# Kernel optimization log

Measured on AMD Instinct MI355X. Metric: run time of the kernel, lower is better.

Reference implementation:

```python
import jax, jax.numpy as jnp
import numpy as np

EPS = 1e-8

def _cosine_weights(keys, M, reverse=False):
    # keys: (bs, r, W); M: (bs, W, N) -> softmax over slots of cosine sim, shape (bs, r, N)
    kn = keys / (jnp.linalg.norm(keys, axis=-1, keepdims=True) + EPS)
    Mn = M / (jnp.linalg.norm(M, axis=1, keepdims=True) + EPS)
    dist = jnp.einsum('brw,bwn->brn', kn, Mn)
    if reverse:
        dist = -dist
    return jax.nn.softmax(dist, axis=2)

def setup_inputs() -> dict:
    key = jax.random.key(0)
    ks = jax.random.split(key, 8)
    bs, W, N, R = 128, 256, 2048, 4
    return {
        'k_r': jax.random.normal(ks[0], (bs, R * W), jnp.float32),
        'm_t': jax.random.normal(ks[1], (bs, W), jnp.float32),
        'e_t': jax.random.normal(ks[2], (bs, W), jnp.float32),
        'm_erased': jax.random.normal(ks[3], (bs, 1, W), jnp.float32),
        'memory': jax.random.uniform(ks[4], (bs, W, N), jnp.float32),
        'gW': jax.random.normal(ks[5], (1, 2 * W), jnp.float32) * 0.05,
        'gb': jnp.zeros((1,), jnp.float32),
        'oW': jax.random.normal(ks[6], (W, 2 * W), jnp.float32) * 0.05,
        'ob': jnp.zeros((W,), jnp.float32),
    }

def reference(k_r, m_t, e_t, m_erased, memory, gW, gb, oW, ob):
    bs, W, N = memory.shape
    R = k_r.shape[1] // W
    read_keys = jnp.tanh(k_r.reshape(bs, R, W))
    write_m = jnp.tanh(m_t.reshape(bs, 1, W))            # m_t candidate (bs,1,W)
    erase_vec = jax.nn.softmax(e_t.reshape(bs, 1, W), axis=2)
    # MixGate(write_m, m_erased)
    cat = jnp.concatenate([write_m, m_erased], axis=-1)  # (bs,1,2W)
    g = jax.nn.sigmoid(jnp.einsum('biw,ow->bio', cat, gW) + gb)  # (bs,1,1)
    gated = jnp.concatenate([g * write_m, (1.0 - g) * m_erased], axis=-1)
    write_key = jax.nn.relu(jnp.einsum('biw,ow->bio', gated, oW) + ob)  # (bs,1,W)
    # content weighting with reversed (dissimilarity) cosine
    write_wt = _cosine_weights(write_key, memory, reverse=True)  # (bs,1,N)
    # M = M * (1 - et^T wt) + mt^T wt
    reset_gate = 1.0 - jnp.einsum('biw,bin->bwn', erase_vec, write_wt)
    M_new = memory * reset_gate + jnp.einsum('biw,bin->bwn', write_m, write_wt)
    # read
    read_wt = _cosine_weights(read_keys, M_new)          # (bs,R,N)
    m_read = jnp.einsum('brn,bwn->brw', read_wt, M_new)  # (bs,R,W)
    return (m_read, M_new, read_wt)
```

## Files before the change

### kernel.cpp

```cpp
#include <hip/hip_runtime.h>
#include <math.h>

#define EPS 1e-8f
#define BS 128
#define W 256
#define N 2048
#define R 4

__device__ inline float wave_sum(float v) {
#pragma unroll
    for (int o = 32; o > 0; o >>= 1) v += __shfl_xor(v, o, 64);
    return v;
}
__device__ inline float wave_max(float v) {
#pragma unroll
    for (int o = 32; o > 0; o >>= 1) v = fmaxf(v, __shfl_xor(v, o, 64));
    return v;
}

__global__ void k_prep(const float* __restrict__ k_r, const float* __restrict__ m_t,
                       const float* __restrict__ e_t, const float* __restrict__ m_er,
                       const float* __restrict__ gW, const float* __restrict__ gb,
                       const float* __restrict__ oW, const float* __restrict__ ob,
                       float* __restrict__ wm_o, float* __restrict__ er_o,
                       float* __restrict__ knw_o, float* __restrict__ knr_o) {
    int b = blockIdx.x, t = threadIdx.x;
    int lane = t & 63, wid = t >> 6;
    __shared__ float red[4];
    __shared__ float gated[2 * W];
    __shared__ float wk_s[W];

    float wm = tanhf(m_t[b * W + t]);
    float me = m_er[b * W + t];
    wm_o[b * W + t] = wm;

    float e = e_t[b * W + t];
    float mx = wave_max(e);
    if (lane == 0) red[wid] = mx;
    __syncthreads();
    mx = fmaxf(fmaxf(red[0], red[1]), fmaxf(red[2], red[3]));
    __syncthreads();
    float ex = expf(e - mx);
    float s = wave_sum(ex);
    if (lane == 0) red[wid] = s;
    __syncthreads();
    s = red[0] + red[1] + red[2] + red[3];
    __syncthreads();
    er_o[b * W + t] = ex / s;

    float p = wm * gW[t] + me * gW[W + t];
    float ps = wave_sum(p);
    if (lane == 0) red[wid] = ps;
    __syncthreads();
    ps = red[0] + red[1] + red[2] + red[3] + gb[0];
    __syncthreads();
    float g = 1.0f / (1.0f + expf(-ps));
    gated[t] = g * wm;
    gated[W + t] = (1.0f - g) * me;
    __syncthreads();

    const float4* g4 = (const float4*)gated;
    float4 g0 = g4[lane];
    float4 g1 = g4[64 + lane];
    for (int i = 0; i < 64; i++) {
        int o = wid * 64 + i;
        const float4* orow = (const float4*)(oW + (size_t)o * 2 * W);
        float4 w0 = orow[lane];
        float4 w1 = orow[64 + lane];
        float pp = w0.x * g0.x + w0.y * g0.y + w0.z * g0.z + w0.w * g0.w
                 + w1.x * g1.x + w1.y * g1.y + w1.z * g1.z + w1.w * g1.w;
        pp = wave_sum(pp);
        if (lane == 0) wk_s[o] = fmaxf(pp + ob[o], 0.0f);
    }
    __syncthreads();
    float wk = wk_s[t];
    float ss = wave_sum(wk * wk);
    if (lane == 0) red[wid] = ss;
    __syncthreads();
    ss = red[0] + red[1] + red[2] + red[3];
    __syncthreads();
    knw_o[b * W + t] = wk / (sqrtf(ss) + EPS);

    for (int r = 0; r < R; r++) {
        float rk = tanhf(k_r[(b * R + r) * W + t]);
        float s2 = wave_sum(rk * rk);
        if (lane == 0) red[wid] = s2;
        __syncthreads();
        s2 = red[0] + red[1] + red[2] + red[3];
        __syncthreads();
        knr_o[(b * R + r) * W + t] = rk / (sqrtf(s2) + EPS);
    }
}

__global__ void k_wdist(const float* __restrict__ mem, const float* __restrict__ knw,
                        float* __restrict__ dist) {
    int b = blockIdx.y;
    int t = threadIdx.x;
    int n4 = blockIdx.x * 256 + t;
    __shared__ float k[W];
    k[t] = knw[b * W + t];
    __syncthreads();
    const float4* base = (const float4*)(mem + (size_t)b * W * N) + n4;
    float4 dot = make_float4(0.f, 0.f, 0.f, 0.f);
    float4 ss = make_float4(0.f, 0.f, 0.f, 0.f);
#pragma unroll 8
    for (int w = 0; w < W; w++) {
        float4 v = base[(size_t)w * (N / 4)];
        float kw = k[w];
        dot.x += kw * v.x; dot.y += kw * v.y; dot.z += kw * v.z; dot.w += kw * v.w;
        ss.x += v.x * v.x; ss.y += v.y * v.y; ss.z += v.z * v.z; ss.w += v.w * v.w;
    }
    float4 o;
    o.x = -(dot.x / (sqrtf(ss.x) + EPS));
    o.y = -(dot.y / (sqrtf(ss.y) + EPS));
    o.z = -(dot.z / (sqrtf(ss.z) + EPS));
    o.w = -(dot.w / (sqrtf(ss.w) + EPS));
    ((float4*)(dist + (size_t)b * N))[n4] = o;
}

__global__ void k_softmax_rows(float* __restrict__ io) {
    int row = blockIdx.x, t = threadIdx.x;
    int lane = t & 63, wid = t >> 6;
    float* p = io + (size_t)row * N;
    __shared__ float red[4];
    float v[8];
    float mx = -INFINITY;
#pragma unroll
    for (int k = 0; k < 8; k++) {
        v[k] = p[t + k * 256];
        mx = fmaxf(mx, v[k]);
    }
    mx = wave_max(mx);
    if (lane == 0) red[wid] = mx;
    __syncthreads();
    mx = fmaxf(fmaxf(red[0], red[1]), fmaxf(red[2], red[3]));
    __syncthreads();
    float s = 0.f;
#pragma unroll
    for (int k = 0; k < 8; k++) {
        v[k] = expf(v[k] - mx);
        s += v[k];
    }
    s = wave_sum(s);
    if (lane == 0) red[wid] = s;
    __syncthreads();
    s = red[0] + red[1] + red[2] + red[3];
    float inv = 1.0f / s;
#pragma unroll
    for (int k = 0; k < 8; k++) p[t + k * 256] = v[k] * inv;
}

__global__ void k_update(const float* __restrict__ mem, const float* __restrict__ wdist,
                         const float* __restrict__ er, const float* __restrict__ wm,
                         const float* __restrict__ knr,
                         float* __restrict__ Mnew, float* __restrict__ dist_r) {
    int b = blockIdx.y;
    int t = threadIdx.x;
    int lane = t & 63, wid = t >> 6;
    int n4 = blockIdx.x * 256 + t;
    __shared__ float se[W], sw[W];
    __shared__ float4 skT[W];
    __shared__ float red[4];
    se[t] = er[b * W + t];
    sw[t] = wm[b * W + t];
    const float* kb = knr + (size_t)b * R * W;
    skT[t] = make_float4(kb[t], kb[W + t], kb[2 * W + t], kb[3 * W + t]);

    const float4* drow4 = (const float4*)(wdist + (size_t)b * N);
    float4 a0 = drow4[t];
    float4 a1 = drow4[256 + t];
    float mx = fmaxf(fmaxf(fmaxf(a0.x, a0.y), fmaxf(a0.z, a0.w)),
                     fmaxf(fmaxf(a1.x, a1.y), fmaxf(a1.z, a1.w)));
    mx = wave_max(mx);
    if (lane == 0) red[wid] = mx;
    __syncthreads();
    mx = fmaxf(fmaxf(red[0], red[1]), fmaxf(red[2], red[3]));
    __syncthreads();
    float sm = expf(a0.x - mx) + expf(a0.y - mx) + expf(a0.z - mx) + expf(a0.w - mx)
             + expf(a1.x - mx) + expf(a1.y - mx) + expf(a1.z - mx) + expf(a1.w - mx);
    sm = wave_sum(sm);
    if (lane == 0) red[wid] = sm;
    __syncthreads();
    sm = red[0] + red[1] + red[2] + red[3];
    float inv = 1.0f / sm;
    float4 dmine = drow4[n4];
    float4 wt;
    wt.x = expf(dmine.x - mx) * inv;
    wt.y = expf(dmine.y - mx) * inv;
    wt.z = expf(dmine.z - mx) * inv;
    wt.w = expf(dmine.w - mx) * inv;

    const float4* mb = (const float4*)(mem + (size_t)b * W * N) + n4;
    float4* ob = (float4*)(Mnew + (size_t)b * W * N) + n4;
    float4 ssv = make_float4(0.f, 0.f, 0.f, 0.f);
    float4 d0 = make_float4(0.f, 0.f, 0.f, 0.f);
    float4 d1 = make_float4(0.f, 0.f, 0.f, 0.f);
    float4 d2 = make_float4(0.f, 0.f, 0.f, 0.f);
    float4 d3 = make_float4(0.f, 0.f, 0.f, 0.f);
#pragma unroll 4
    for (int w = 0; w < W; w++) {
        float4 v = mb[(size_t)w * (N / 4)];
        float ew = se[w], mw = sw[w];
        float4 mn;
        mn.x = v.x + wt.x * (mw - v.x * ew);
        mn.y = v.y + wt.y * (mw - v.y * ew);
        mn.z = v.z + wt.z * (mw - v.z * ew);
        mn.w = v.w + wt.w * (mw - v.w * ew);
        ob[(size_t)w * (N / 4)] = mn;
        ssv.x += mn.x * mn.x; ssv.y += mn.y * mn.y;
        ssv.z += mn.z * mn.z; ssv.w += mn.w * mn.w;
        float4 kv = skT[w];
        d0.x += kv.x * mn.x; d0.y += kv.x * mn.y; d0.z += kv.x * mn.z; d0.w += kv.x * mn.w;
        d1.x += kv.y * mn.x; d1.y += kv.y * mn.y; d1.z += kv.y * mn.z; d1.w += kv.y * mn.w;
        d2.x += kv.z * mn.x; d2.y += kv.z * mn.y; d2.z += kv.z * mn.z; d2.w += kv.z * mn.w;
        d3.x += kv.w * mn.x; d3.y += kv.w * mn.y; d3.z += kv.w * mn.z; d3.w += kv.w * mn.w;
    }
    float4 ivn;
    ivn.x = 1.0f / (sqrtf(ssv.x) + EPS);
    ivn.y = 1.0f / (sqrtf(ssv.y) + EPS);
    ivn.z = 1.0f / (sqrtf(ssv.z) + EPS);
    ivn.w = 1.0f / (sqrtf(ssv.w) + EPS);
    float4* dr = (float4*)(dist_r + (size_t)b * R * N);
    dr[0 * (N / 4) + n4] = make_float4(d0.x * ivn.x, d0.y * ivn.y, d0.z * ivn.z, d0.w * ivn.w);
    dr[1 * (N / 4) + n4] = make_float4(d1.x * ivn.x, d1.y * ivn.y, d1.z * ivn.z, d1.w * ivn.w);
    dr[2 * (N / 4) + n4] = make_float4(d2.x * ivn.x, d2.y * ivn.y, d2.z * ivn.z, d2.w * ivn.w);
    dr[3 * (N / 4) + n4] = make_float4(d3.x * ivn.x, d3.y * ivn.y, d3.z * ivn.z, d3.w * ivn.w);
}

__global__ void k_mread(const float* __restrict__ Mnew, const float* __restrict__ rwt_g,
                        float* __restrict__ m_read) {
    int b = blockIdx.y;
    int w0 = blockIdx.x * 64;
    int t = threadIdx.x;
    int lane = t & 63, wid = t >> 6;
    int half = wid & 1, rowgrp = wid >> 1;
    int fbase = half * 256 + lane;

    float4 rw[R][4];
#pragma unroll
    for (int r = 0; r < R; r++) {
        const float4* rrow = (const float4*)(rwt_g + ((size_t)b * R + r) * N);
#pragma unroll
        for (int k = 0; k < 4; k++) rw[r][k] = rrow[fbase + k * 64];
    }

    __shared__ float part[64][2][4];
    const float* Mb = Mnew + (size_t)b * W * N;
#pragma unroll 2
    for (int wi = 0; wi < 32; wi++) {
        int wl = rowgrp * 32 + wi;
        const float4* mrow = (const float4*)(Mb + (size_t)(w0 + wl) * N);
        float4 v[4];
#pragma unroll
        for (int k = 0; k < 4; k++) v[k] = mrow[fbase + k * 64];
        float a0 = 0.f, a1 = 0.f, a2 = 0.f, a3 = 0.f;
#pragma unroll
        for (int k = 0; k < 4; k++) {
            a0 += rw[0][k].x * v[k].x + rw[0][k].y * v[k].y + rw[0][k].z * v[k].z + rw[0][k].w * v[k].w;
            a1 += rw[1][k].x * v[k].x + rw[1][k].y * v[k].y + rw[1][k].z * v[k].z + rw[1][k].w * v[k].w;
            a2 += rw[2][k].x * v[k].x + rw[2][k].y * v[k].y + rw[2][k].z * v[k].z + rw[2][k].w * v[k].w;
            a3 += rw[3][k].x * v[k].x + rw[3][k].y * v[k].y + rw[3][k].z * v[k].z + rw[3][k].w * v[k].w;
        }
        a0 = wave_sum(a0);
        a1 = wave_sum(a1);
        a2 = wave_sum(a2);
        a3 = wave_sum(a3);
        if (lane == 0) {
            part[wl][half][0] = a0;
            part[wl][half][1] = a1;
            part[wl][half][2] = a2;
            part[wl][half][3] = a3;
        }
    }
    __syncthreads();
    int w = t >> 2, r = t & 3;
    float sres = part[w][0][r] + part[w][1][r];
    m_read[((size_t)b * R + r) * W + w0 + w] = sres;
}

extern "C" void kernel_launch(void* const* d_in, const int* in_sizes, int n_in,
                              void* d_out, int out_size, void* d_ws, size_t ws_size,
                              hipStream_t stream) {
    const float* k_r  = (const float*)d_in[0];
    const float* m_t  = (const float*)d_in[1];
    const float* e_t  = (const float*)d_in[2];
    const float* m_er = (const float*)d_in[3];
    const float* mem  = (const float*)d_in[4];
    const float* gW   = (const float*)d_in[5];
    const float* gb   = (const float*)d_in[6];
    const float* oW   = (const float*)d_in[7];
    const float* ob   = (const float*)d_in[8];

    float* out = (float*)d_out;
    float* m_read = out;
    float* Mnew   = out + (size_t)BS * R * W;
    float* rwt    = out + (size_t)BS * R * W + (size_t)BS * W * N;

    float* ws  = (float*)d_ws;
    float* wm  = ws;
    float* er  = ws + (size_t)BS * W;
    float* knw = ws + (size_t)2 * BS * W;
    float* knr = ws + (size_t)3 * BS * W;
    float* wdist = ws + (size_t)3 * BS * W + (size_t)BS * R * W;

    k_prep<<<BS, 256, 0, stream>>>(k_r, m_t, e_t, m_er, gW, gb, oW, ob, wm, er, knw, knr);
    k_wdist<<<dim3(2, BS), 256, 0, stream>>>(mem, knw, wdist);
    k_update<<<dim3(2, BS), 256, 0, stream>>>(mem, wdist, er, wm, knr, Mnew, rwt);
    k_softmax_rows<<<BS * R, 256, 0, stream>>>(rwt);
    k_mread<<<dim3(4, BS), 256, 0, stream>>>(Mnew, rwt, m_read);
}
```

Before: 259.2 us.

## Split W reduction across two thread halves in wdist and update kernels

```diff
diff --git a/kernel.cpp b/kernel.cpp
--- a/kernel.cpp
+++ b/kernel.cpp
@@ -92,30 +92,42 @@
     }
 }
 
-__global__ void k_wdist(const float* __restrict__ mem, const float* __restrict__ knw,
-                        float* __restrict__ dist) {
+__global__ void __launch_bounds__(256, 2)
+k_wdist(const float* __restrict__ mem, const float* __restrict__ knw,
+        float* __restrict__ dist) {
     int b = blockIdx.y;
     int t = threadIdx.x;
-    int n4 = blockIdx.x * 256 + t;
+    int half = t >> 7, c = t & 127;
+    int n4 = blockIdx.x * 128 + c;
     __shared__ float k[W];
+    __shared__ float4 pdot[128], pss[128];
     k[t] = knw[b * W + t];
     __syncthreads();
     const float4* base = (const float4*)(mem + (size_t)b * W * N) + n4;
     float4 dot = make_float4(0.f, 0.f, 0.f, 0.f);
     float4 ss = make_float4(0.f, 0.f, 0.f, 0.f);
+    int w0 = half * 128;
 #pragma unroll 8
-    for (int w = 0; w < W; w++) {
+    for (int i = 0; i < 128; i++) {
+        int w = w0 + i;
         float4 v = base[(size_t)w * (N / 4)];
         float kw = k[w];
         dot.x += kw * v.x; dot.y += kw * v.y; dot.z += kw * v.z; dot.w += kw * v.w;
         ss.x += v.x * v.x; ss.y += v.y * v.y; ss.z += v.z * v.z; ss.w += v.w * v.w;
     }
-    float4 o;
-    o.x = -(dot.x / (sqrtf(ss.x) + EPS));
-    o.y = -(dot.y / (sqrtf(ss.y) + EPS));
-    o.z = -(dot.z / (sqrtf(ss.z) + EPS));
-    o.w = -(dot.w / (sqrtf(ss.w) + EPS));
-    ((float4*)(dist + (size_t)b * N))[n4] = o;
+    if (half == 0) { pdot[c] = dot; pss[c] = ss; }
+    __syncthreads();
+    if (half == 1) {
+        float4 od = pdot[c], os = pss[c];
+        dot.x += od.x; dot.y += od.y; dot.z += od.z; dot.w += od.w;
+        ss.x += os.x; ss.y += os.y; ss.z += os.z; ss.w += os.w;
+        float4 o;
+        o.x = -(dot.x / (sqrtf(ss.x) + EPS));
+        o.y = -(dot.y / (sqrtf(ss.y) + EPS));
+        o.z = -(dot.z / (sqrtf(ss.z) + EPS));
+        o.w = -(dot.w / (sqrtf(ss.w) + EPS));
+        ((float4*)(dist + (size_t)b * N))[n4] = o;
+    }
 }
 
 __global__ void k_softmax_rows(float* __restrict__ io) {
@@ -150,17 +162,20 @@
     for (int k = 0; k < 8; k++) p[t + k * 256] = v[k] * inv;
 }
 
-__global__ void k_update(const float* __restrict__ mem, const float* __restrict__ wdist,
-                         const float* __restrict__ er, const float* __restrict__ wm,
-                         const float* __restrict__ knr,
-                         float* __restrict__ Mnew, float* __restrict__ dist_r) {
+__global__ void __launch_bounds__(256, 2)
+k_update(const float* __restrict__ mem, const float* __restrict__ wdist,
+         const float* __restrict__ er, const float* __restrict__ wm,
+         const float* __restrict__ knr,
+         float* __restrict__ Mnew, float* __restrict__ dist_r) {
     int b = blockIdx.y;
     int t = threadIdx.x;
     int lane = t & 63, wid = t >> 6;
-    int n4 = blockIdx.x * 256 + t;
+    int half = t >> 7, c = t & 127;
+    int n4 = blockIdx.x * 128 + c;
     __shared__ float se[W], sw[W];
     __shared__ float4 skT[W];
     __shared__ float red[4];
+    __shared__ float4 pd0[128], pd1[128], pd2[128], pd3[128], pssv[128];
     se[t] = er[b * W + t];
     sw[t] = wm[b * W + t];
     const float* kb = knr + (size_t)b * R * W;
@@ -197,8 +212,10 @@
     float4 d1 = make_float4(0.f, 0.f, 0.f, 0.f);
     float4 d2 = make_float4(0.f, 0.f, 0.f, 0.f);
     float4 d3 = make_float4(0.f, 0.f, 0.f, 0.f);
-#pragma unroll 4
-    for (int w = 0; w < W; w++) {
+    int w0 = half * 128;
+#pragma unroll 8
+    for (int i = 0; i < 128; i++) {
+        int w = w0 + i;
         float4 v = mb[(size_t)w * (N / 4)];
         float ew = se[w], mw = sw[w];
         float4 mn;
@@ -215,20 +232,33 @@
         d2.x += kv.z * mn.x; d2.y += kv.z * mn.y; d2.z += kv.z * mn.z; d2.w += kv.z * mn.w;
         d3.x += kv.w * mn.x; d3.y += kv.w * mn.y; d3.z += kv.w * mn.z; d3.w += kv.w * mn.w;
     }
-    float4 ivn;
-    ivn.x = 1.0f / (sqrtf(ssv.x) + EPS);
-    ivn.y = 1.0f / (sqrtf(ssv.y) + EPS);
-    ivn.z = 1.0f / (sqrtf(ssv.z) + EPS);
-    ivn.w = 1.0f / (sqrtf(ssv.w) + EPS);
-    float4* dr = (float4*)(dist_r + (size_t)b * R * N);
-    dr[0 * (N / 4) + n4] = make_float4(d0.x * ivn.x, d0.y * ivn.y, d0.z * ivn.z, d0.w * ivn.w);
-    dr[1 * (N / 4) + n4] = make_float4(d1.x * ivn.x, d1.y * ivn.y, d1.z * ivn.z, d1.w * ivn.w);
-    dr[2 * (N / 4) + n4] = make_float4(d2.x * ivn.x, d2.y * ivn.y, d2.z * ivn.z, d2.w * ivn.w);
-    dr[3 * (N / 4) + n4] = make_float4(d3.x * ivn.x, d3.y * ivn.y, d3.z * ivn.z, d3.w * ivn.w);
-}
-
-__global__ void k_mread(const float* __restrict__ Mnew, const float* __restrict__ rwt_g,
-                        float* __restrict__ m_read) {
+    if (half == 0) {
+        pd0[c] = d0; pd1[c] = d1; pd2[c] = d2; pd3[c] = d3; pssv[c] = ssv;
+    }
+    __syncthreads();
+    if (half == 1) {
+        float4 q;
+        q = pd0[c]; d0.x += q.x; d0.y += q.y; d0.z += q.z; d0.w += q.w;
+        q = pd1[c]; d1.x += q.x; d1.y += q.y; d1.z += q.z; d1.w += q.w;
+        q = pd2[c]; d2.x += q.x; d2.y += q.y; d2.z += q.z; d2.w += q.w;
+        q = pd3[c]; d3.x += q.x; d3.y += q.y; d3.z += q.z; d3.w += q.w;
+        q = pssv[c]; ssv.x += q.x; ssv.y += q.y; ssv.z += q.z; ssv.w += q.w;
+        float4 ivn;
+        ivn.x = 1.0f / (sqrtf(ssv.x) + EPS);
+        ivn.y = 1.0f / (sqrtf(ssv.y) + EPS);
+        ivn.z = 1.0f / (sqrtf(ssv.z) + EPS);
+        ivn.w = 1.0f / (sqrtf(ssv.w) + EPS);
+        float4* dr = (float4*)(dist_r + (size_t)b * R * N);
+        dr[0 * (N / 4) + n4] = make_float4(d0.x * ivn.x, d0.y * ivn.y, d0.z * ivn.z, d0.w * ivn.w);
+        dr[1 * (N / 4) + n4] = make_float4(d1.x * ivn.x, d1.y * ivn.y, d1.z * ivn.z, d1.w * ivn.w);
+        dr[2 * (N / 4) + n4] = make_float4(d2.x * ivn.x, d2.y * ivn.y, d2.z * ivn.z, d2.w * ivn.w);
+        dr[3 * (N / 4) + n4] = make_float4(d3.x * ivn.x, d3.y * ivn.y, d3.z * ivn.z, d3.w * ivn.w);
+    }
+}
+
+__global__ void __launch_bounds__(256, 2)
+k_mread(const float* __restrict__ Mnew, const float* __restrict__ rwt_g,
+        float* __restrict__ m_read) {
     int b = blockIdx.y;
     int w0 = blockIdx.x * 64;
     int t = threadIdx.x;
@@ -246,7 +276,7 @@
 
     __shared__ float part[64][2][4];
     const float* Mb = Mnew + (size_t)b * W * N;
-#pragma unroll 2
+#pragma unroll 4
     for (int wi = 0; wi < 32; wi++) {
         int wl = rowgrp * 32 + wi;
         const float4* mrow = (const float4*)(Mb + (size_t)(w0 + wl) * N);
@@ -304,8 +334,8 @@
     float* wdist = ws + (size_t)3 * BS * W + (size_t)BS * R * W;
 
     k_prep<<<BS, 256, 0, stream>>>(k_r, m_t, e_t, m_er, gW, gb, oW, ob, wm, er, knw, knr);
-    k_wdist<<<dim3(2, BS), 256, 0, stream>>>(mem, knw, wdist);
-    k_update<<<dim3(2, BS), 256, 0, stream>>>(mem, wdist, er, wm, knr, Mnew, rwt);
+    k_wdist<<<dim3(4, BS), 256, 0, stream>>>(mem, knw, wdist);
+    k_update<<<dim3(4, BS), 256, 0, stream>>>(mem, wdist, er, wm, knr, Mnew, rwt);
     k_softmax_rows<<<BS * R, 256, 0, stream>>>(rwt);
     k_mread<<<dim3(4, BS), 256, 0, stream>>>(Mnew, rwt, m_read);
 }
```

Measured after the change: 267.9 us. 3.4% more time.

## Compute read distances algebraically from memory moments, fusing update and read

Applied to the files above, without the earlier changes.

```diff
diff --git a/kernel.cpp b/kernel.cpp
--- a/kernel.cpp
+++ b/kernel.cpp
@@ -5,7 +5,10 @@
 #define BS 128
 #define W 256
 #define N 2048
+#define N4 (N / 4)
 #define R 4
+
+using v4f = float __attribute__((ext_vector_type(4)));
 
 __device__ inline float wave_sum(float v) {
 #pragma unroll
@@ -16,6 +19,28 @@
 #pragma unroll
     for (int o = 32; o > 0; o >>= 1) v = fmaxf(v, __shfl_xor(v, o, 64));
     return v;
+}
+__device__ inline float block_sum(float v, volatile float* red, int lane, int wid) {
+    v = wave_sum(v);
+    if (lane == 0) red[wid] = v;
+    __syncthreads();
+    v = red[0] + red[1] + red[2] + red[3];
+    __syncthreads();
+    return v;
+}
+__device__ inline float block_max(float v, volatile float* red, int lane, int wid) {
+    v = wave_max(v);
+    if (lane == 0) red[wid] = v;
+    __syncthreads();
+    v = fmaxf(fmaxf(red[0], red[1]), fmaxf(red[2], red[3]));
+    __syncthreads();
+    return v;
+}
+__device__ inline void fma4s(float4& a, float s, const float4& v) {
+    a.x += s * v.x; a.y += s * v.y; a.z += s * v.z; a.w += s * v.w;
+}
+__device__ inline void fma44(float4& a, const float4& u, const float4& v) {
+    a.x += u.x * v.x; a.y += u.y * v.y; a.z += u.z * v.z; a.w += u.w * v.w;
 }
 
 __global__ void k_prep(const float* __restrict__ k_r, const float* __restrict__ m_t,
@@ -23,7 +48,8 @@
                        const float* __restrict__ gW, const float* __restrict__ gb,
                        const float* __restrict__ oW, const float* __restrict__ ob,
                        float* __restrict__ wm_o, float* __restrict__ er_o,
-                       float* __restrict__ knw_o, float* __restrict__ knr_o) {
+                       float* __restrict__ knw_o, float* __restrict__ knr_o,
+                       float* __restrict__ c0_o) {
     int b = blockIdx.x, t = threadIdx.x;
     int lane = t & 63, wid = t >> 6;
     __shared__ float red[4];
@@ -35,25 +61,16 @@
     wm_o[b * W + t] = wm;
 
     float e = e_t[b * W + t];
-    float mx = wave_max(e);
-    if (lane == 0) red[wid] = mx;
-    __syncthreads();
-    mx = fmaxf(fmaxf(red[0], red[1]), fmaxf(red[2], red[3]));
-    __syncthreads();
+    float mx = block_max(e, red, lane, wid);
     float ex = expf(e - mx);
-    float s = wave_sum(ex);
-    if (lane == 0) red[wid] = s;
-    __syncthreads();
-    s = red[0] + red[1] + red[2] + red[3];
-    __syncthreads();
+    float s = block_sum(ex, red, lane, wid);
     er_o[b * W + t] = ex / s;
 
+    float pw = block_sum(wm * wm, red, lane, wid);
+    if (t == 0) c0_o[b * 5 + 4] = pw;
+
     float p = wm * gW[t] + me * gW[W + t];
-    float ps = wave_sum(p);
-    if (lane == 0) red[wid] = ps;
-    __syncthreads();
-    ps = red[0] + red[1] + red[2] + red[3] + gb[0];
-    __syncthreads();
+    float ps = block_sum(p, red, lane, wid) + gb[0];
     float g = 1.0f / (1.0f + expf(-ps));
     gated[t] = g * wm;
     gated[W + t] = (1.0f - g) * me;
@@ -74,208 +91,277 @@
     }
     __syncthreads();
     float wk = wk_s[t];
-    float ss = wave_sum(wk * wk);
-    if (lane == 0) red[wid] = ss;
-    __syncthreads();
-    ss = red[0] + red[1] + red[2] + red[3];
-    __syncthreads();
+    float ss = block_sum(wk * wk, red, lane, wid);
     knw_o[b * W + t] = wk / (sqrtf(ss) + EPS);
 
     for (int r = 0; r < R; r++) {
         float rk = tanhf(k_r[(b * R + r) * W + t]);
-        float s2 = wave_sum(rk * rk);
-        if (lane == 0) red[wid] = s2;
-        __syncthreads();
-        s2 = red[0] + red[1] + red[2] + red[3];
-        __syncthreads();
-        knr_o[(b * R + r) * W + t] = rk / (sqrtf(s2) + EPS);
-    }
-}
-
-__global__ void k_wdist(const float* __restrict__ mem, const float* __restrict__ knw,
-                        float* __restrict__ dist) {
-    int b = blockIdx.y;
+        float s2 = block_sum(rk * rk, red, lane, wid);
+        float kn = rk / (sqrtf(s2) + EPS);
+        knr_o[(b * R + r) * W + t] = kn;
+        float c0 = block_sum(kn * wm, red, lane, wid);
+        if (t == 0) c0_o[b * 5 + r] = c0;
+    }
+}
+
+__global__ void __launch_bounds__(256, 2)
+k_moments(const float* __restrict__ mem, const float* __restrict__ knw_g,
+          const float* __restrict__ er_g, const float* __restrict__ wm_g,
+          const float* __restrict__ knr_g, float4* __restrict__ scr) {
+    int b = blockIdx.y, bx = blockIdx.x;
     int t = threadIdx.x;
-    int n4 = blockIdx.x * 256 + t;
-    __shared__ float k[W];
-    k[t] = knw[b * W + t];
-    __syncthreads();
+    int half = t >> 7, c = t & 127;
+    int n4 = bx * 128 + c;
+    __shared__ float knw_s[W], er_s[W], wm_s[W], knr_s[R * W];
+    __shared__ float4 comb[128 * 7];
+
+    knw_s[t] = knw_g[b * W + t];
+    er_s[t]  = er_g[b * W + t];
+    wm_s[t]  = wm_g[b * W + t];
+#pragma unroll
+    for (int r = 0; r < R; r++) knr_s[r * W + t] = knr_g[(b * R + r) * W + t];
+    __syncthreads();
+
+    float4 acc[14];
+#pragma unroll
+    for (int j = 0; j < 14; j++) acc[j] = make_float4(0.f, 0.f, 0.f, 0.f);
+
     const float4* base = (const float4*)(mem + (size_t)b * W * N) + n4;
-    float4 dot = make_float4(0.f, 0.f, 0.f, 0.f);
-    float4 ss = make_float4(0.f, 0.f, 0.f, 0.f);
-#pragma unroll 8
-    for (int w = 0; w < W; w++) {
-        float4 v = base[(size_t)w * (N / 4)];
-        float kw = k[w];
-        dot.x += kw * v.x; dot.y += kw * v.y; dot.z += kw * v.z; dot.w += kw * v.w;
-        ss.x += v.x * v.x; ss.y += v.y * v.y; ss.z += v.z * v.z; ss.w += v.w * v.w;
-    }
-    float4 o;
-    o.x = -(dot.x / (sqrtf(ss.x) + EPS));
-    o.y = -(dot.y / (sqrtf(ss.y) + EPS));
-    o.z = -(dot.z / (sqrtf(ss.z) + EPS));
-    o.w = -(dot.w / (sqrtf(ss.w) + EPS));
-    ((float4*)(dist + (size_t)b * N))[n4] = o;
-}
-
-__global__ void k_softmax_rows(float* __restrict__ io) {
-    int row = blockIdx.x, t = threadIdx.x;
-    int lane = t & 63, wid = t >> 6;
-    float* p = io + (size_t)row * N;
-    __shared__ float red[4];
-    float v[8];
-    float mx = -INFINITY;
-#pragma unroll
-    for (int k = 0; k < 8; k++) {
-        v[k] = p[t + k * 256];
-        mx = fmaxf(mx, v[k]);
-    }
-    mx = wave_max(mx);
-    if (lane == 0) red[wid] = mx;
-    __syncthreads();
-    mx = fmaxf(fmaxf(red[0], red[1]), fmaxf(red[2], red[3]));
-    __syncthreads();
-    float s = 0.f;
-#pragma unroll
-    for (int k = 0; k < 8; k++) {
-        v[k] = expf(v[k] - mx);
-        s += v[k];
-    }
-    s = wave_sum(s);
-    if (lane == 0) red[wid] = s;
-    __syncthreads();
-    s = red[0] + red[1] + red[2] + red[3];
-    float inv = 1.0f / s;
-#pragma unroll
-    for (int k = 0; k < 8; k++) p[t + k * 256] = v[k] * inv;
-}
-
-__global__ void k_update(const float* __restrict__ mem, const float* __restrict__ wdist,
-                         const float* __restrict__ er, const float* __restrict__ wm,
-                         const float* __restrict__ knr,
-                         float* __restrict__ Mnew, float* __restrict__ dist_r) {
-    int b = blockIdx.y;
+    int w0 = half * 128;
+#pragma unroll 4
+    for (int i = 0; i < 128; i++) {
+        int w = w0 + i;
+        float4 v = base[(size_t)w * N4];
+        float e = er_s[w], m = wm_s[w], kw = knw_s[w];
+        float4 ev;
+        ev.x = e * v.x; ev.y = e * v.y; ev.z = e * v.z; ev.w = e * v.w;
+        fma4s(acc[0], kw, v);
+        fma44(acc[1], v, v);
+        fma44(acc[2], ev, v);
+        fma44(acc[3], ev, ev);
+        fma4s(acc[4], m, v);
+        fma4s(acc[5], m, ev);
+        fma4s(acc[6], knr_s[w], v);
+        fma4s(acc[7], knr_s[W + w], v);
+        fma4s(acc[8], knr_s[2 * W + w], v);
+        fma4s(acc[9], knr_s[3 * W + w], v);
+        fma4s(acc[10], knr_s[w], ev);
+        fma4s(acc[11], knr_s[W + w], ev);
+        fma4s(acc[12], knr_s[2 * W + w], ev);
+        fma4s(acc[13], knr_s[3 * W + w], ev);
+    }
+
+    if (half == 0) {
+#pragma unroll
+        for (int j = 0; j < 7; j++) comb[c * 7 + j] = acc[j];
+    }
+    __syncthreads();
+    if (half == 1) {
+#pragma unroll
+        for (int j = 0; j < 7; j++) {
+            float4 q = comb[c * 7 + j];
+            q.x += acc[j].x; q.y += acc[j].y; q.z += acc[j].z; q.w += acc[j].w;
+            scr[((size_t)(b * 14 + j)) * N4 + n4] = q;
+        }
+    }
+    __syncthreads();
+    if (half == 0) {
+#pragma unroll
+        for (int j = 0; j < 7; j++) comb[c * 7 + j] = acc[7 + j];
+    }
+    __syncthreads();
+    if (half == 1) {
+#pragma unroll
+        for (int j = 0; j < 7; j++) {
+            float4 q = comb[c * 7 + j];
+            q.x += acc[7 + j].x; q.y += acc[7 + j].y; q.z += acc[7 + j].z; q.w += acc[7 + j].w;
+            scr[((size_t)(b * 14 + 7 + j)) * N4 + n4] = q;
+        }
+    }
+}
+
+__global__ void k_weights(const float4* __restrict__ scr, const float* __restrict__ c0_g,
+                          float* __restrict__ wwt_g, float* __restrict__ rwt_out,
+                          float* __restrict__ C_g) {
+    int b = blockIdx.y, pair = blockIdx.x;
     int t = threadIdx.x;
     int lane = t & 63, wid = t >> 6;
-    int n4 = blockIdx.x * 256 + t;
-    __shared__ float se[W], sw[W];
-    __shared__ float4 skT[W];
     __shared__ float red[4];
-    se[t] = er[b * W + t];
-    sw[t] = wm[b * W + t];
-    const float* kb = knr + (size_t)b * R * W;
-    skT[t] = make_float4(kb[t], kb[W + t], kb[2 * W + t], kb[3 * W + t]);
-
-    const float4* drow4 = (const float4*)(wdist + (size_t)b * N);
-    float4 a0 = drow4[t];
-    float4 a1 = drow4[256 + t];
-    float mx = fmaxf(fmaxf(fmaxf(a0.x, a0.y), fmaxf(a0.z, a0.w)),
-                     fmaxf(fmaxf(a1.x, a1.y), fmaxf(a1.z, a1.w)));
-    mx = wave_max(mx);
-    if (lane == 0) red[wid] = mx;
-    __syncthreads();
-    mx = fmaxf(fmaxf(red[0], red[1]), fmaxf(red[2], red[3]));
-    __syncthreads();
-    float sm = expf(a0.x - mx) + expf(a0.y - mx) + expf(a0.z - mx) + expf(a0.w - mx)
-             + expf(a1.x - mx) + expf(a1.y - mx) + expf(a1.z - mx) + expf(a1.w - mx);
-    sm = wave_sum(sm);
-    if (lane == 0) red[wid] = sm;
-    __syncthreads();
-    sm = red[0] + red[1] + red[2] + red[3];
-    float inv = 1.0f / sm;
-    float4 dmine = drow4[n4];
-    float4 wt;
-    wt.x = expf(dmine.x - mx) * inv;
-    wt.y = expf(dmine.y - mx) * inv;
-    wt.z = expf(dmine.z - mx) * inv;
-    wt.w = expf(dmine.w - mx) * inv;
-
-    const float4* mb = (const float4*)(mem + (size_t)b * W * N) + n4;
-    float4* ob = (float4*)(Mnew + (size_t)b * W * N) + n4;
-    float4 ssv = make_float4(0.f, 0.f, 0.f, 0.f);
-    float4 d0 = make_float4(0.f, 0.f, 0.f, 0.f);
-    float4 d1 = make_float4(0.f, 0.f, 0.f, 0.f);
-    float4 d2 = make_float4(0.f, 0.f, 0.f, 0.f);
-    float4 d3 = make_float4(0.f, 0.f, 0.f, 0.f);
-#pragma unroll 4
-    for (int w = 0; w < W; w++) {
-        float4 v = mb[(size_t)w * (N / 4)];
-        float ew = se[w], mw = sw[w];
-        float4 mn;
-        mn.x = v.x + wt.x * (mw - v.x * ew);
-        mn.y = v.y + wt.y * (mw - v.y * ew);
-        mn.z = v.z + wt.z * (mw - v.z * ew);
-        mn.w = v.w + wt.w * (mw - v.w * ew);
-        ob[(size_t)w * (N / 4)] = mn;
-        ssv.x += mn.x * mn.x; ssv.y += mn.y * mn.y;
-        ssv.z += mn.z * mn.z; ssv.w += mn.w * mn.w;
-        float4 kv = skT[w];
-        d0.x += kv.x * mn.x; d0.y += kv.x * mn.y; d0.z += kv.x * mn.z; d0.w += kv.x * mn.w;
-        d1.x += kv.y * mn.x; d1.y += kv.y * mn.y; d1.z += kv.y * mn.z; d1.w += kv.y * mn.w;
-        d2.x += kv.z * mn.x; d2.y += kv.z * mn.y; d2.z += kv.z * mn.z; d2.w += kv.z * mn.w;
-        d3.x += kv.w * mn.x; d3.y += kv.w * mn.y; d3.z += kv.w * mn.z; d3.w += kv.w * mn.w;
-    }
-    float4 ivn;
-    ivn.x = 1.0f / (sqrtf(ssv.x) + EPS);
-    ivn.y = 1.0f / (sqrtf(ssv.y) + EPS);
-    ivn.z = 1.0f / (sqrtf(ssv.z) + EPS);
-    ivn.w = 1.0f / (sqrtf(ssv.w) + EPS);
-    float4* dr = (float4*)(dist_r + (size_t)b * R * N);
-    dr[0 * (N / 4) + n4] = make_float4(d0.x * ivn.x, d0.y * ivn.y, d0.z * ivn.z, d0.w * ivn.w);
-    dr[1 * (N / 4) + n4] = make_float4(d1.x * ivn.x, d1.y * ivn.y, d1.z * ivn.z, d1.w * ivn.w);
-    dr[2 * (N / 4) + n4] = make_float4(d2.x * ivn.x, d2.y * ivn.y, d2.z * ivn.z, d2.w * ivn.w);
-    dr[3 * (N / 4) + n4] = make_float4(d3.x * ivn.x, d3.y * ivn.y, d3.z * ivn.z, d3.w * ivn.w);
-}
-
-__global__ void k_mread(const float* __restrict__ Mnew, const float* __restrict__ rwt_g,
-                        float* __restrict__ m_read) {
+
+    const float4* S0 = scr + (size_t)(b * 14) * N4;
+    float4 s1a = S0[t],        ssa = S0[N4 + t];
+    float4 s1b = S0[256 + t],  ssb = S0[N4 + 256 + t];
+
+    float4 da, db;
+    da.x = -(s1a.x / (sqrtf(ssa.x) + EPS)); da.y = -(s1a.y / (sqrtf(ssa.y) + EPS));
+    da.z = -(s1a.z / (sqrtf(ssa.z) + EPS)); da.w = -(s1a.w / (sqrtf(ssa.w) + EPS));
+    db.x = -(s1b.x / (sqrtf(ssb.x) + EPS)); db.y = -(s1b.y / (sqrtf(ssb.y) + EPS));
+    db.z = -(s1b.z / (sqrtf(ssb.z) + EPS)); db.w = -(s1b.w / (sqrtf(ssb.w) + EPS));
+
+    float m8 = fmaxf(fmaxf(fmaxf(da.x, da.y), fmaxf(da.z, da.w)),
+                     fmaxf(fmaxf(db.x, db.y), fmaxf(db.z, db.w)));
+    float mx = block_max(m8, red, lane, wid);
+    float4 ea, eb;
+    ea.x = expf(da.x - mx); ea.y = expf(da.y - mx); ea.z = expf(da.z - mx); ea.w = expf(da.w - mx);
+    eb.x = expf(db.x - mx); eb.y = expf(db.y - mx); eb.z = expf(db.z - mx); eb.w = expf(db.w - mx);
+    float s8 = ea.x + ea.y + ea.z + ea.w + eb.x + eb.y + eb.z + eb.w;
+    float Z = block_sum(s8, red, lane, wid);
+    float inv = 1.0f / Z;
+    float4 ua, ub;
+    ua.x = ea.x * inv; ua.y = ea.y * inv; ua.z = ea.z * inv; ua.w = ea.w * inv;
+    ub.x = eb.x * inv; ub.y = eb.y * inv; ub.z = eb.z * inv; ub.w = eb.w * inv;
+    if (pair == 0) {
+        ((float4*)(wwt_g + (size_t)b * N))[t] = ua;
+        ((float4*)(wwt_g + (size_t)b * N))[256 + t] = ub;
+    }
+
+    float4 q1a = S0[2 * N4 + t], q2a = S0[3 * N4 + t], p0a = S0[4 * N4 + t], p1a = S0[5 * N4 + t];
+    float4 q1b = S0[2 * N4 + 256 + t], q2b = S0[3 * N4 + 256 + t],
+           p0b = S0[4 * N4 + 256 + t], p1b = S0[5 * N4 + 256 + t];
+    float pw = c0_g[b * 5 + 4];
+
+    float4 dena, denb;
+    {
+        dena.x = sqrtf(ssa.x + ua.x * (2.f * p0a.x - 2.f * q1a.x) + ua.x * ua.x * (q2a.x - 2.f * p1a.x + pw)) + EPS;
+        dena.y = sqrtf(ssa.y + ua.y * (2.f * p0a.y - 2.f * q1a.y) + ua.y * ua.y * (q2a.y - 2.f * p1a.y + pw)) + EPS;
+        dena.z = sqrtf(ssa.z + ua.z * (2.f * p0a.z - 2.f * q1a.z) + ua.z * ua.z * (q2a.z - 2.f * p1a.z + pw)) + EPS;
+        dena.w = sqrtf(ssa.w + ua.w * (2.f * p0a.w - 2.f * q1a.w) + ua.w * ua.w * (q2a.w - 2.f * p1a.w + pw)) + EPS;
+        denb.x = sqrtf(ssb.x + ub.x * (2.f * p0b.x - 2.f * q1b.x) + ub.x * ub.x * (q2b.x - 2.f * p1b.x + pw)) + EPS;
+        denb.y = sqrtf(ssb.y + ub.y * (2.f * p0b.y - 2.f * q1b.y) + ub.y * ub.y * (q2b.y - 2.f * p1b.y + pw)) + EPS;
+        denb.z = sqrtf(ssb.z + ub.z * (2.f * p0b.z - 2.f * q1b.z) + ub.z * ub.z * (q2b.z - 2.f * p1b.z + pw)) + EPS;
+        denb.w = sqrtf(ssb.w + ub.w * (2.f * p0b.w - 2.f * q1b.w) + ub.w * ub.w * (q2b.w - 2.f * p1b.w + pw)) + EPS;
+    }
+
+#pragma unroll
+    for (int rr = 0; rr < 2; rr++) {
+        int r = pair * 2 + rr;
+        float c0 = c0_g[b * 5 + r];
+        float4 t0a = S0[(6 + r) * N4 + t], t1a = S0[(10 + r) * N4 + t];
+        float4 t0b = S0[(6 + r) * N4 + 256 + t], t1b = S0[(10 + r) * N4 + 256 + t];
+        float4 dra, drb;
+        dra.x = (t0a.x + ua.x * (c0 - t1a.x)) / dena.x;
+        dra.y = (t0a.y + ua.y * (c0 - t1a.y)) / dena.y;
+        dra.z = (t0a.z + ua.z * (c0 - t1a.z)) / dena.z;
+        dra.w = (t0a.w + ua.w * (c0 - t1a.w)) / dena.w;
+        drb.x = (t0b.x + ub.x * (c0 - t1b.x)) / denb.x;
+        drb.y = (t0b.y + ub.y * (c0 - t1b.y)) / denb.y;
+        drb.z = (t0b.z + ub.z * (c0 - t1b.z)) / denb.z;
+        drb.w = (t0b.w + ub.w * (c0 - t1b.w)) / denb.w;
+
+        float rm = fmaxf(fmaxf(fmaxf(dra.x, dra.y), fmaxf(dra.z, dra.w)),
+                         fmaxf(fmaxf(drb.x, drb.y), fmaxf(drb.z, drb.w)));
+        float rmx = block_max(rm, red, lane, wid);
+        float4 ra, rb;
+        ra.x = expf(dra.x - rmx); ra.y = expf(dra.y - rmx);
+        ra.z = expf(dra.z - rmx); ra.w = expf(dra.w - rmx);
+        rb.x = expf(drb.x - rmx); rb.y = expf(drb.y - rmx);
+        rb.z = expf(drb.z - rmx); rb.w = expf(drb.w - rmx);
+        float rs = ra.x + ra.y + ra.z + ra.w + rb.x + rb.y + rb.z + rb.w;
+        float RZ = block_sum(rs, red, lane, wid);
+        float rinv = 1.0f / RZ;
+        ra.x *= rinv; ra.y *= rinv; ra.z *= rinv; ra.w *= rinv;
+        rb.x *= rinv; rb.y *= rinv; rb.z *= rinv; rb.w *= rinv;
+        float4* ro = (float4*)(rwt_out + (size_t)b * R * N);
+        ro[r * 512 + t] = ra;
+        ro[r * 512 + 256 + t] = rb;
+        float cpart = ra.x * ua.x + ra.y * ua.y + ra.z * ua.z + ra.w * ua.w
+                    + rb.x * ub.x + rb.y * ub.y + rb.z * ub.z + rb.w * ub.w;
+        float C = block_sum(cpart, red, lane, wid);
+        if (t == 0) C_g[b * R + r] = C;
+    }
+}
+
+__global__ void __launch_bounds__(256, 2)
+k_mnew_read(const float* __restrict__ mem, const float* __restrict__ wwt_g,
+            const float* __restrict__ rwt_g, const float* __restrict__ C_g,
+            const float* __restrict__ er_g, const float* __restrict__ wm_g,
+            float* __restrict__ Mnew, float* __restrict__ m_read) {
     int b = blockIdx.y;
     int w0 = blockIdx.x * 64;
     int t = threadIdx.x;
     int lane = t & 63, wid = t >> 6;
+
+    __shared__ float4 rwt4[R * 512];
+    __shared__ float4 wwt4[512];
+    __shared__ float er_s[64], wm_s[64];
+    __shared__ float part_a[64][2][4], part_b[64][2][4];
+
+    const float4* ro = (const float4*)(rwt_g + (size_t)b * R * N);
+#pragma unroll
+    for (int i = 0; i < 8; i++) rwt4[i * 256 + t] = ro[i * 256 + t];
+    const float4* wo = (const float4*)(wwt_g + (size_t)b * N);
+    wwt4[t] = wo[t];
+    wwt4[256 + t] = wo[256 + t];
+    if (t < 64) {
+        er_s[t] = er_g[b * W + w0 + t];
+        wm_s[t] = wm_g[b * W + w0 + t];
+    }
+    __syncthreads();
+
     int half = wid & 1, rowgrp = wid >> 1;
     int fbase = half * 256 + lane;
 
-    float4 rw[R][4];
-#pragma unroll
-    for (int r = 0; r < R; r++) {
-        const float4* rrow = (const float4*)(rwt_g + ((size_t)b * R + r) * N);
-#pragma unroll
-        for (int k = 0; k < 4; k++) rw[r][k] = rrow[fbase + k * 64];
-    }
-
-    __shared__ float part[64][2][4];
-    const float* Mb = Mnew + (size_t)b * W * N;
+    float4 wt4[4], rw[R][4], uw[R][4];
+#pragma unroll
+    for (int k = 0; k < 4; k++) wt4[k] = wwt4[fbase + k * 64];
+#pragma unroll
+    for (int r = 0; r < R; r++)
+#pragma unroll
+        for (int k = 0; k < 4; k++) {
+            rw[r][k] = rwt4[r * 512 + fbase + k * 64];
+            uw[r][k].x = rw[r][k].x * wt4[k].x;
+            uw[r][k].y = rw[r][k].y * wt4[k].y;
+            uw[r][k].z = rw[r][k].z * wt4[k].z;
+            uw[r][k].w = rw[r][k].w * wt4[k].w;
+        }
+
+    const float* Mb = mem + (size_t)b * W * N;
+    float* Ob = Mnew + (size_t)b * W * N;
 #pragma unroll 2
     for (int wi = 0; wi < 32; wi++) {
         int wl = rowgrp * 32 + wi;
+        float erw = er_s[wl], wmw = wm_s[wl];
         const float4* mrow = (const float4*)(Mb + (size_t)(w0 + wl) * N);
+        v4f* orow = (v4f*)(Ob + (size_t)(w0 + wl) * N);
         float4 v[4];
 #pragma unroll
         for (int k = 0; k < 4; k++) v[k] = mrow[fbase + k * 64];
         float a0 = 0.f, a1 = 0.f, a2 = 0.f, a3 = 0.f;
+        float b0 = 0.f, b1 = 0.f, b2 = 0.f, b3 = 0.f;
 #pragma unroll
         for (int k = 0; k < 4; k++) {
+            v4f mn;
+            mn[0] = v[k].x + wt4[k].x * (wmw - v[k].x * erw);
+            mn[1] = v[k].y + wt4[k].y * (wmw - v[k].y * erw);
+            mn[2] = v[k].z + wt4[k].z * (wmw - v[k].z * erw);
+            mn[3] = v[k].w + wt4[k].w * (wmw - v[k].w * erw);
+            __builtin_nontemporal_store(mn, orow + fbase + k * 64);
             a0 += rw[0][k].x * v[k].x + rw[0][k].y * v[k].y + rw[0][k].z * v[k].z + rw[0][k].w * v[k].w;
             a1 += rw[1][k].x * v[k].x + rw[1][k].y * v[k].y + rw[1][k].z * v[k].z + rw[1][k].w * v[k].w;
             a2 += rw[2][k].x * v[k].x + rw[2][k].y * v[k].y + rw[2][k].z * v[k].z + rw[2][k].w * v[k].w;
             a3 += rw[3][k].x * v[k].x + rw[3][k].y * v[k].y + rw[3][k].z * v[k].z + rw[3][k].w * v[k].w;
+            b0 += uw[0][k].x * v[k].x + uw[0][k].y * v[k].y + uw[0][k].z * v[k].z + uw[0][k].w * v[k].w;
+            b1 += uw[1][k].x * v[k].x + uw[1][k].y * v[k].y + uw[1][k].z * v[k].z + uw[1][k].w * v[k].w;
+            b2 += uw[2][k].x * v[k].x + uw[2][k].y * v[k].y + uw[2][k].z * v[k].z + uw[2][k].w * v[k].w;
+            b3 += uw[3][k].x * v[k].x + uw[3][k].y * v[k].y + uw[3][k].z * v[k].z + uw[3][k].w * v[k].w;
         }
-        a0 = wave_sum(a0);
-        a1 = wave_sum(a1);
-        a2 = wave_sum(a2);
-        a3 = wave_sum(a3);
+        a0 = wave_sum(a0); a1 = wave_sum(a1); a2 = wave_sum(a2); a3 = wave_sum(a3);
+        b0 = wave_sum(b0); b1 = wave_sum(b1); b2 = wave_sum(b2); b3 = wave_sum(b3);
         if (lane == 0) {
-            part[wl][half][0] = a0;
-            part[wl][half][1] = a1;
-            part[wl][half][2] = a2;
-            part[wl][half][3] = a3;
+            part_a[wl][half][0] = a0; part_a[wl][half][1] = a1;
+            part_a[wl][half][2] = a2; part_a[wl][half][3] = a3;
+            part_b[wl][half][0] = b0; part_b[wl][half][1] = b1;
+            part_b[wl][half][2] = b2; part_b[wl][half][3] = b3;
         }
     }
     __syncthreads();
     int w = t >> 2, r = t & 3;
-    float sres = part[w][0][r] + part[w][1][r];
-    m_read[((size_t)b * R + r) * W + w0 + w] = sres;
+    float A = part_a[w][0][r] + part_a[w][1][r];
+    float B = part_b[w][0][r] + part_b[w][1][r];
+    float C = C_g[b * R + r];
+    float erv = er_s[w];
+    float wmv = wm_s[w];
+    m_read[((size_t)b * R + r) * W + w0 + w] = A - erv * B + wmv * C;
 }
 
 extern "C" void kernel_launch(void* const* d_in, const int* in_sizes, int n_in,
@@ -296,16 +382,21 @@
     float* Mnew   = out + (size_t)BS * R * W;
     float* rwt    = out + (size_t)BS * R * W + (size_t)BS * W * N;
 
+    float4* scr = (float4*)Mnew;
+
     float* ws  = (float*)d_ws;
     float* wm  = ws;
-    float* er  = ws + (size_t)BS * W;
-    float* knw = ws + (size_t)2 * BS * W;
-    float* knr = ws + (size_t)3 * BS * W;
-    float* wdist = ws + (size_t)3 * BS * W + (size_t)BS * R * W;
-
-    k_prep<<<BS, 256, 0, stream>>>(k_r, m_t, e_t, m_er, gW, gb, oW, ob, wm, er, knw, knr);
-    k_wdist<<<dim3(2, BS), 256, 0, stream>>>(mem, knw, wdist);
-    k_update<<<dim3(2, BS), 256, 0, stream>>>(mem, wdist, er, wm, knr, Mnew, rwt);
-    k_softmax_rows<<<BS * R, 256, 0, stream>>>(rwt);
-    k_mread<<<dim3(4, BS), 256, 0, stream>>>(Mnew, rwt, m_read);
-}
+    float* er  = wm + (size_t)BS * W;
+    float* knw = er + (size_t)BS * W;
+    float* knr = knw + (size_t)BS * W;
+    float* c0  = knr + (size_t)BS * R * W;
+    float* wwt = c0 + (size_t)BS * 8;
+    float* Cg  = wwt + (size_t)BS * N;
+
+    k_prep<<<BS, 256, 0, stream>>>(k_r, m_t, e_t, m_er, gW, gb, oW, ob,
+                                   wm, er, knw, knr, c0);
+    k_moments<<<dim3(4, BS), 256, 0, stream>>>(mem, knw, er, wm, knr, scr);
+    k_weights<<<dim3(2, BS), 256, 0, stream>>>(scr, c0, wwt, rwt, Cg);
+    k_mnew_read<<<dim3(4, BS), 256, 0, stream>>>(mem, wwt, rwt, Cg, er, wm,
+                                                 Mnew, m_read);
+}
```

After: 208.5 us. 19.6% less time.
